# Kernel tuning notes

Hardware: AMD Instinct MI355X
Metric: run time of the kernel (lower is better)

Reference implementation:

```python
import jax, jax.numpy as jnp
import numpy as np

N, S, L, E, H = 8, 2, 512, 1024, 16
D = E // H  # head_dim = 64


def setup_inputs() -> dict:
    key = jax.random.key(0)
    ks = jax.random.split(key, 10)
    inp = {
        "values": jax.random.normal(ks[0], (N, S, L, E), dtype=jnp.float32),
        "keys": jax.random.normal(ks[1], (N, S, L, E), dtype=jnp.float32),
        "query": jax.random.normal(ks[2], (N, S, L, E), dtype=jnp.float32),
        "mask": jax.random.randint(ks[3], (N, S, L, 1), 0, 2, dtype=jnp.int32),
        # per-head projection weights, nn.Linear(D, D, bias=False): y = x @ W.T
        "Wv": jax.random.normal(ks[4], (D, D), dtype=jnp.float32) / np.sqrt(D),
        "Wk": jax.random.normal(ks[5], (D, D), dtype=jnp.float32) / np.sqrt(D),
        "Wq": jax.random.normal(ks[6], (D, D), dtype=jnp.float32) / np.sqrt(D),
        # output projection nn.Linear(E, E)
        "Wo": jax.random.normal(ks[7], (E, E), dtype=jnp.float32) / np.sqrt(E),
        "bo": jax.random.normal(ks[8], (E,), dtype=jnp.float32) * 0.01,
    }
    return inp


def reference(values, keys, query, mask, Wv, Wk, Wq, Wo, bo):
    n, s, l, e = query.shape
    h, d = H, D
    key_len = keys.shape[2]
    # split heads: (n, s, len, h, d)
    v = values.reshape(n, s, l, h, d) @ Wv.T
    k = keys.reshape(n, s, l, h, d) @ Wk.T
    q = query.reshape(n, s, l, h, d) @ Wq.T
    # energy: (n, s, h, q_len, k_len)
    energy = jnp.einsum('nsqhd,nskhd->nshqk', q, k)
    # mask[:, :, :, 0] masks QUERY positions (broadcast over heads and k)
    m = mask[:, :, :, 0]  # (n, s, l)
    energy = jnp.where(m[:, :, None, :, None] == 0, jnp.float32(-1e20), energy)
    # NOTE: softmax over the QUERY axis (dim=3), faithful to the original
    attn = jax.nn.softmax(energy / jnp.sqrt(jnp.float32(key_len)), axis=3)
    out = jnp.einsum('nshql,nslhd->nsqhd', attn, v)
    out = out.reshape(n, s, l, h * d)
    return out @ Wo.T + bo
```

## Files before the change

### kernel.cpp

```cpp
#include <hip/hip_runtime.h>
#include <math.h>

#define LL 512
#define EE 1024
#define HH 16
#define DD 64
#define NSX 16
#define NT (NSX*LL)
#define NSLE (NT*EE)
#define SCALE_Q 0.06375871f

typedef unsigned short u16;
typedef short bf16x8 __attribute__((ext_vector_type(8)));
typedef float f32x4 __attribute__((ext_vector_type(4)));

__device__ inline u16 f2bf(float f) {
  unsigned u = __float_as_uint(f);
  u += 0x7fff + ((u >> 16) & 1);
  return (u16)(u >> 16);
}

#define FEXP2(x) __builtin_amdgcn_exp2f(x)
#define MFMA32(a, b, c) __builtin_amdgcn_mfma_f32_16x16x32_bf16((a), (b), (c), 0, 0, 0)

__device__ inline void gload16(const void* g, void* l) {
  __builtin_amdgcn_global_load_lds(
      (const __attribute__((address_space(1))) unsigned int*)g,
      (__attribute__((address_space(3))) unsigned int*)l, 16, 0, 0);
}

__global__ void __launch_bounds__(256) convw_kernel(
    const float* __restrict__ Wv, const float* __restrict__ Wk,
    const float* __restrict__ Wq, const float* __restrict__ Wo,
    u16* __restrict__ Wvb, u16* __restrict__ Wkb,
    u16* __restrict__ Wqb, u16* __restrict__ Wob) {
  int i = blockIdx.x * 256 + threadIdx.x;
  const float* s; u16* d; int j;
  if (i < 262144) { s = Wo; d = Wob; j = i; }
  else {
    j = i - 262144;
    if (j < 1024)      { s = Wv; d = Wvb; }
    else if (j < 2048) { s = Wk; d = Wkb; j -= 1024; }
    else               { s = Wq; d = Wqb; j -= 2048; }
  }
  float4 f = ((const float4*)s)[j];
  ushort4 o; o.x = f2bf(f.x); o.y = f2bf(f.y); o.z = f2bf(f.z); o.w = f2bf(f.w);
  ((ushort4*)d)[j] = o;
}

__global__ void __launch_bounds__(256) proj_kernel(
    const float* __restrict__ vals, const float* __restrict__ keys,
    const float* __restrict__ qry,
    const u16* __restrict__ Wvb, const u16* __restrict__ Wkb,
    const u16* __restrict__ Wqb,
    u16* __restrict__ vpT, u16* __restrict__ kp, u16* __restrict__ qp) {
  const int b = blockIdx.x;
  const int tt0 = b & 7, hg = (b >> 3) & 3, ns = (b >> 5) & 15, mat = b >> 9;
  const int tid = threadIdx.x;
  const int wid = tid >> 6, lane = tid & 63, quad = lane >> 4, l16 = lane & 15;
  const int h = hg*4 + wid;
  const float* src = (mat == 0 ? vals : mat == 1 ? keys : qry);
  const u16*   W   = (mat == 0 ? Wvb  : mat == 1 ? Wkb  : Wqb);
  u16* dst = (mat == 1 ? kp : qp);
  const float sc = (mat == 2) ? SCALE_Q : 1.f;
  bf16x8 wf[4][2];
  #pragma unroll
  for (int nt = 0; nt < 4; ++nt) {
    wf[nt][0] = *(const bf16x8*)&W[(nt*16 + l16)*DD + quad*8];
    wf[nt][1] = *(const bf16x8*)&W[(nt*16 + l16)*DD + 32 + quad*8];
  }
  f32x4 z = {0.f, 0.f, 0.f, 0.f};
  const float* xr0 = src + (size_t)(ns*LL + tt0*16 + l16)*EE + h*DD;
  const float* xr1 = xr0 + (size_t)128*EE;
  float4 x0 = *(const float4*)&xr0[quad*8];
  float4 x1 = *(const float4*)&xr0[quad*8 + 4];
  float4 x2 = *(const float4*)&xr0[32 + quad*8];
  float4 x3 = *(const float4*)&xr0[32 + quad*8 + 4];
  float4 y0 = *(const float4*)&xr1[quad*8];
  float4 y1 = *(const float4*)&xr1[quad*8 + 4];
  float4 y2 = *(const float4*)&xr1[32 + quad*8];
  float4 y3 = *(const float4*)&xr1[32 + quad*8 + 4];
  #pragma unroll
  for (int j = 0; j < 4; ++j) {
    const int tt = tt0 + 8*j;
    const int t0 = ns*LL + tt*16;
    float4 n0, n1, n2, n3;
    if (j < 2) {
      const float* xrn = src + (size_t)(t0 + 256 + l16)*EE + h*DD;
      n0 = *(const float4*)&xrn[quad*8];
      n1 = *(const float4*)&xrn[quad*8 + 4];
      n2 = *(const float4*)&xrn[32 + quad*8];
      n3 = *(const float4*)&xrn[32 + quad*8 + 4];
    }
    bf16x8 af0, af1;
    af0[0] = (short)f2bf(x0.x); af0[1] = (short)f2bf(x0.y);
    af0[2] = (short)f2bf(x0.z); af0[3] = (short)f2bf(x0.w);
    af0[4] = (short)f2bf(x1.x); af0[5] = (short)f2bf(x1.y);
    af0[6] = (short)f2bf(x1.z); af0[7] = (short)f2bf(x1.w);
    af1[0] = (short)f2bf(x2.x); af1[1] = (short)f2bf(x2.y);
    af1[2] = (short)f2bf(x2.z); af1[3] = (short)f2bf(x2.w);
    af1[4] = (short)f2bf(x3.x); af1[5] = (short)f2bf(x3.y);
    af1[6] = (short)f2bf(x3.z); af1[7] = (short)f2bf(x3.w);
    if (mat == 0) {
      f32x4 acc[4];
      #pragma unroll
      for (int nt = 0; nt < 4; ++nt) {
        acc[nt] = MFMA32(af0, wf[nt][0], z);
        acc[nt] = MFMA32(af1, wf[nt][1], acc[nt]);
      }
      #pragma unroll
      for (int nt = 0; nt < 4; ++nt) {
        ushort4 o;
        o.x = f2bf(acc[nt][0]); o.y = f2bf(acc[nt][1]);
        o.z = f2bf(acc[nt][2]); o.w = f2bf(acc[nt][3]);
        size_t idx = ((size_t)((ns*HH + h)*DD + nt*16 + l16))*LL + tt*16 + quad*4;
        *(ushort4*)&vpT[idx] = o;
      }
    } else {
      f32x4 acc[4];
      #pragma unroll
      for (int nt = 0; nt < 4; ++nt) {
        acc[nt] = MFMA32(wf[nt][0], af0, z);
        acc[nt] = MFMA32(wf[nt][1], af1, acc[nt]);
      }
      #pragma unroll
      for (int nt = 0; nt < 4; ++nt) {
        ushort4 o;
        o.x = f2bf(acc[nt][0] * sc); o.y = f2bf(acc[nt][1] * sc);
        o.z = f2bf(acc[nt][2] * sc); o.w = f2bf(acc[nt][3] * sc);
        *(ushort4*)&dst[(size_t)(t0 + l16)*EE + h*DD + nt*16 + quad*4] = o;
      }
    }
    x0 = y0; x1 = y1; x2 = y2; x3 = y3;
    if (j < 2) { y0 = n0; y1 = n1; y2 = n2; y3 = n3; }
  }
}

__global__ void __launch_bounds__(1024, 4) attn_kernel(
    const u16* __restrict__ qp, const u16* __restrict__ kp,
    const u16* __restrict__ vpT, const int* __restrict__ mask,
    u16* __restrict__ oat) {
  const int b = blockIdx.x;
  const int h = b & 15, ns = b >> 4;
  const int tid = threadIdx.x;
  const int wid = tid >> 6, lane = tid & 63, quad = lane >> 4, l16 = lane & 15;
  __shared__ u16 Ks[LL][72];
  __shared__ u16 Vt[2][DD][72];
  __shared__ u16 pt[16][32][40];
  __shared__ float csum[LL];
  float* psum = (float*)pt;
  const size_t kgbase = ((size_t)(ns*LL))*EE + h*DD;
  for (int i = tid; i < 4096; i += 1024) {
    int row = i >> 3, seg = (i & 7) * 8;
    *(bf16x8*)&Ks[row][seg] = *(const bf16x8*)&kp[kgbase + (size_t)row*EE + seg];
  }
  const int q0 = wid*32;
  bf16x8 qf[2][2];
  float maf[2][4];
  #pragma unroll
  for (int qt = 0; qt < 2; ++qt) {
    const u16* qrow = qp + ((size_t)(ns*LL + q0 + qt*16 + l16))*EE + h*DD;
    qf[qt][0] = *(const bf16x8*)&qrow[quad*8];
    qf[qt][1] = *(const bf16x8*)&qrow[32 + quad*8];
    #pragma unroll
    for (int r = 0; r < 4; ++r)
      maf[qt][r] = mask[ns*LL + q0 + qt*16 + quad*4 + r] ? 1.f : 0.f;
  }
  f32x4 z = {0.f, 0.f, 0.f, 0.f};
  __syncthreads();
  for (int lt = 0; lt < 32; ++lt) {
    bf16x8 kf0 = *(const bf16x8*)&Ks[lt*16 + l16][quad*8];
    bf16x8 kf1 = *(const bf16x8*)&Ks[lt*16 + l16][32 + quad*8];
    float part = 0.f;
    #pragma unroll
    for (int qt = 0; qt < 2; ++qt) {
      __builtin_amdgcn_s_setprio(1);
      f32x4 e = MFMA32(qf[qt][0], kf0, z);
      e = MFMA32(qf[qt][1], kf1, e);
      __builtin_amdgcn_s_setprio(0);
      #pragma unroll
      for (int r = 0; r < 4; ++r)
        part += maf[qt][r] * FEXP2(e[r]);
    }
    part += __shfl_xor(part, 16);
    part += __shfl_xor(part, 32);
    if (quad == 0) psum[wid*512 + lt*16 + l16] = part;
  }
  __syncthreads();
  if (tid < LL) {
    float s = 0.f;
    #pragma unroll
    for (int w = 0; w < 16; ++w) s += psum[w*512 + tid];
    csum[tid] = (s > 0.f) ? 1.f/s : 0.f;
  }
  __syncthreads();
  f32x4 acc[4][2] = {{z,z},{z,z},{z,z},{z,z}};
  const size_t vgbase = ((size_t)((ns*HH + h)*DD))*LL;
  for (int lc = 0; lc < 8; ++lc) {
    if (tid < 512) {
      int row = tid >> 3, seg = (tid & 7) * 8;
      *(bf16x8*)&Vt[lc & 1][row][seg] =
          *(const bf16x8*)&vpT[vgbase + (size_t)row*LL + lc*64 + seg];
    }
    __syncthreads();
    #pragma unroll
    for (int lt2 = 0; lt2 < 4; ++lt2) {
      const int lrow = lc*64 + lt2*16 + l16;
      bf16x8 kf0 = *(const bf16x8*)&Ks[lrow][quad*8];
      bf16x8 kf1 = *(const bf16x8*)&Ks[lrow][32 + quad*8];
      const float csv = csum[lrow];
      #pragma unroll
      for (int qt = 0; qt < 2; ++qt) {
        __builtin_amdgcn_s_setprio(1);
        f32x4 e = MFMA32(qf[qt][0], kf0, z);
        e = MFMA32(qf[qt][1], kf1, e);
        __builtin_amdgcn_s_setprio(0);
        #pragma unroll
        for (int r = 0; r < 4; ++r)
          pt[wid][qt*16 + quad*4 + r][lt2 & 1 ? 16 + l16 : l16] =
              f2bf(maf[qt][r] * csv * FEXP2(e[r]));
        if (lt2 & 1) {
          bf16x8 pa = *(const bf16x8*)&pt[wid][qt*16 + l16][quad*8];
          __builtin_amdgcn_s_setprio(1);
          #pragma unroll
          for (int dt = 0; dt < 4; ++dt) {
            bf16x8 vb = *(const bf16x8*)&Vt[lc & 1][dt*16 + l16]
                                        [(lt2 >> 1)*32 + quad*8];
            acc[dt][qt] = MFMA32(pa, vb, acc[dt][qt]);
          }
          __builtin_amdgcn_s_setprio(0);
        }
      }
    }
  }
  #pragma unroll
  for (int qt = 0; qt < 2; ++qt)
    #pragma unroll
    for (int dt = 0; dt < 4; ++dt)
      #pragma unroll
      for (int r = 0; r < 4; ++r)
        oat[((size_t)(ns*LL + q0 + qt*16 + quad*4 + r))*EE + h*DD + dt*16 + l16] =
            f2bf(acc[dt][qt][r]);
}

__global__ void __launch_bounds__(256) out_gemm_kernel(
    const u16* __restrict__ A, const u16* __restrict__ Wob,
    const float* __restrict__ bo, float* __restrict__ Y) {
  __shared__ u16 As[128][64];
  __shared__ u16 Bs[128][64];
  const int b = blockIdx.x;
  const int nb = b & 7, mb = b >> 3;
  const int m0 = mb*128, n0 = nb*128;
  const int tid = threadIdx.x;
  const int wid = tid >> 6, lane = tid & 63, quad = lane >> 4, l16 = lane & 15;
  const int wm = (wid >> 1)*64, wn = (wid & 1)*64;
  const int r0 = tid >> 3, sseg = (tid & 7) * 8;
  u16* adst = &As[0][0] + tid*8;
  u16* bdst = &Bs[0][0] + tid*8;
  f32x4 z = {0.f, 0.f, 0.f, 0.f};
  f32x4 acc[4][4];
  #pragma unroll
  for (int i = 0; i < 4; ++i)
    #pragma unroll
    for (int j = 0; j < 4; ++j) acc[i][j] = z;
  for (int k0 = 0; k0 < EE; k0 += 64) {
    __syncthreads();
    #pragma unroll
    for (int it = 0; it < 4; ++it) {
      gload16(&A  [(size_t)(m0 + it*32 + r0)*EE + k0 + sseg], adst + it*2048);
      gload16(&Wob[(size_t)(n0 + it*32 + r0)*EE + k0 + sseg], bdst + it*2048);
    }
    __syncthreads();
    #pragma unroll
    for (int kk = 0; kk < 2; ++kk) {
      bf16x8 af[4], bfr[4];
      #pragma unroll
      for (int i = 0; i < 4; ++i)
        af[i] = *(const bf16x8*)&As[wm + i*16 + l16][kk*32 + quad*8];
      #pragma unroll
      for (int j = 0; j < 4; ++j)
        bfr[j] = *(const bf16x8*)&Bs[wn + j*16 + l16][kk*32 + quad*8];
      #pragma unroll
      for (int i = 0; i < 4; ++i)
        #pragma unroll
        for (int j = 0; j < 4; ++j)
          acc[i][j] = MFMA32(af[i], bfr[j], acc[i][j]);
    }
  }
  #pragma unroll
  for (int i = 0; i < 4; ++i)
    #pragma unroll
    for (int j = 0; j < 4; ++j) {
      int col = n0 + wn + j*16 + l16;
      float bias = bo[col];
      #pragma unroll
      for (int r = 0; r < 4; ++r)
        Y[(size_t)(m0 + wm + i*16 + quad*4 + r)*EE + col] = acc[i][j][r] + bias;
    }
}

extern "C" void kernel_launch(void* const* d_in, const int* in_sizes, int n_in,
                              void* d_out, int out_size, void* d_ws, size_t ws_size,
                              hipStream_t stream) {
  const float* values = (const float*)d_in[0];
  const float* keysp  = (const float*)d_in[1];
  const float* query  = (const float*)d_in[2];
  const int*   mask   = (const int*)d_in[3];
  const float* Wv = (const float*)d_in[4];
  const float* Wk = (const float*)d_in[5];
  const float* Wq = (const float*)d_in[6];
  const float* Wo = (const float*)d_in[7];
  const float* bo = (const float*)d_in[8];
  float* Y = (float*)d_out;

  u16* qp  = (u16*)d_ws;
  u16* kp  = qp + NSLE;
  u16* vpT = kp + NSLE;
  u16* oat = vpT + NSLE;
  u16* Wob = oat + NSLE;
  u16* Wvb = Wob + EE*EE;
  u16* Wkb = Wvb + DD*DD;
  u16* Wqb = Wkb + DD*DD;

  convw_kernel<<<1036, 256, 0, stream>>>(Wv, Wk, Wq, Wo, Wvb, Wkb, Wqb, Wob);
  proj_kernel<<<3*NSX*4*8, 256, 0, stream>>>(values, keysp, query,
                                             Wvb, Wkb, Wqb, vpT, kp, qp);
  attn_kernel<<<NSX*HH, 1024, 0, stream>>>(qp, kp, vpT, mask, oat);
  out_gemm_kernel<<<(NT/128)*(EE/128), 256, 0, stream>>>(oat, Wob, bo, Y);
}
```

Baseline: 232.8 us.

## Transpose score MFMA for vectorized P stores, drop setprio, shrink out-GEMM N tile

In the attention kernel, the second-pass score MFMA now has its operands swapped so each lane holds four consecutive key columns for one query row. This lets the probabilities be written to LDS as a single ushort4 and the column sums read as one float4, replacing scalar scattered stores. The s_setprio hints around the MFMAs are removed. The output GEMM tile shrinks from 128x128 to 128x64, doubling the block count (1024 blocks) to improve occupancy and CU coverage at the cost of more A-tile reloads.

```diff
diff --git a/kernel.cpp b/kernel.cpp
--- a/kernel.cpp
+++ b/kernel.cpp
@@ -157,6 +157,7 @@
   const int q0 = wid*32;
   bf16x8 qf[2][2];
   float maf[2][4];
+  float mqf[2];
   #pragma unroll
   for (int qt = 0; qt < 2; ++qt) {
     const u16* qrow = qp + ((size_t)(ns*LL + q0 + qt*16 + l16))*EE + h*DD;
@@ -165,6 +166,7 @@
     #pragma unroll
     for (int r = 0; r < 4; ++r)
       maf[qt][r] = mask[ns*LL + q0 + qt*16 + quad*4 + r] ? 1.f : 0.f;
+    mqf[qt] = mask[ns*LL + q0 + qt*16 + l16] ? 1.f : 0.f;
   }
   f32x4 z = {0.f, 0.f, 0.f, 0.f};
   __syncthreads();
@@ -174,10 +176,8 @@
     float part = 0.f;
     #pragma unroll
     for (int qt = 0; qt < 2; ++qt) {
-      __builtin_amdgcn_s_setprio(1);
       f32x4 e = MFMA32(qf[qt][0], kf0, z);
       e = MFMA32(qf[qt][1], kf1, e);
-      __builtin_amdgcn_s_setprio(0);
       #pragma unroll
       for (int r = 0; r < 4; ++r)
         part += maf[qt][r] * FEXP2(e[r]);
@@ -205,30 +205,29 @@
     __syncthreads();
     #pragma unroll
     for (int lt2 = 0; lt2 < 4; ++lt2) {
-      const int lrow = lc*64 + lt2*16 + l16;
-      bf16x8 kf0 = *(const bf16x8*)&Ks[lrow][quad*8];
-      bf16x8 kf1 = *(const bf16x8*)&Ks[lrow][32 + quad*8];
-      const float csv = csum[lrow];
+      const int lb = lc*64 + lt2*16;
+      bf16x8 kf0 = *(const bf16x8*)&Ks[lb + l16][quad*8];
+      bf16x8 kf1 = *(const bf16x8*)&Ks[lb + l16][32 + quad*8];
+      float4 cs4 = *(const float4*)&csum[lb + quad*4];
       #pragma unroll
       for (int qt = 0; qt < 2; ++qt) {
-        __builtin_amdgcn_s_setprio(1);
-        f32x4 e = MFMA32(qf[qt][0], kf0, z);
-        e = MFMA32(qf[qt][1], kf1, e);
-        __builtin_amdgcn_s_setprio(0);
-        #pragma unroll
-        for (int r = 0; r < 4; ++r)
-          pt[wid][qt*16 + quad*4 + r][lt2 & 1 ? 16 + l16 : l16] =
-              f2bf(maf[qt][r] * csv * FEXP2(e[r]));
+        f32x4 e = MFMA32(kf0, qf[qt][0], z);
+        e = MFMA32(kf1, qf[qt][1], e);
+        const float m = mqf[qt];
+        ushort4 o;
+        o.x = f2bf(m * cs4.x * FEXP2(e[0]));
+        o.y = f2bf(m * cs4.y * FEXP2(e[1]));
+        o.z = f2bf(m * cs4.z * FEXP2(e[2]));
+        o.w = f2bf(m * cs4.w * FEXP2(e[3]));
+        *(ushort4*)&pt[wid][qt*16 + l16][(lt2 & 1)*16 + quad*4] = o;
         if (lt2 & 1) {
           bf16x8 pa = *(const bf16x8*)&pt[wid][qt*16 + l16][quad*8];
-          __builtin_amdgcn_s_setprio(1);
           #pragma unroll
           for (int dt = 0; dt < 4; ++dt) {
             bf16x8 vb = *(const bf16x8*)&Vt[lc & 1][dt*16 + l16]
                                         [(lt2 >> 1)*32 + quad*8];
             acc[dt][qt] = MFMA32(pa, vb, acc[dt][qt]);
           }
-          __builtin_amdgcn_s_setprio(0);
         }
       }
     }
@@ -247,50 +246,51 @@
     const u16* __restrict__ A, const u16* __restrict__ Wob,
     const float* __restrict__ bo, float* __restrict__ Y) {
   __shared__ u16 As[128][64];
-  __shared__ u16 Bs[128][64];
+  __shared__ u16 Bs[64][64];
   const int b = blockIdx.x;
-  const int nb = b & 7, mb = b >> 3;
-  const int m0 = mb*128, n0 = nb*128;
+  const int nb = b & 15, mb = b >> 4;
+  const int m0 = mb*128, n0 = nb*64;
   const int tid = threadIdx.x;
   const int wid = tid >> 6, lane = tid & 63, quad = lane >> 4, l16 = lane & 15;
-  const int wm = (wid >> 1)*64, wn = (wid & 1)*64;
+  const int wm = (wid >> 1)*64, wn = (wid & 1)*32;
   const int r0 = tid >> 3, sseg = (tid & 7) * 8;
   u16* adst = &As[0][0] + tid*8;
   u16* bdst = &Bs[0][0] + tid*8;
   f32x4 z = {0.f, 0.f, 0.f, 0.f};
-  f32x4 acc[4][4];
+  f32x4 acc[4][2];
   #pragma unroll
   for (int i = 0; i < 4; ++i)
     #pragma unroll
-    for (int j = 0; j < 4; ++j) acc[i][j] = z;
+    for (int j = 0; j < 2; ++j) acc[i][j] = z;
   for (int k0 = 0; k0 < EE; k0 += 64) {
     __syncthreads();
     #pragma unroll
-    for (int it = 0; it < 4; ++it) {
-      gload16(&A  [(size_t)(m0 + it*32 + r0)*EE + k0 + sseg], adst + it*2048);
+    for (int it = 0; it < 4; ++it)
+      gload16(&A[(size_t)(m0 + it*32 + r0)*EE + k0 + sseg], adst + it*2048);
+    #pragma unroll
+    for (int it = 0; it < 2; ++it)
       gload16(&Wob[(size_t)(n0 + it*32 + r0)*EE + k0 + sseg], bdst + it*2048);
-    }
     __syncthreads();
     #pragma unroll
     for (int kk = 0; kk < 2; ++kk) {
-      bf16x8 af[4], bfr[4];
+      bf16x8 af[4], bfr[2];
       #pragma unroll
       for (int i = 0; i < 4; ++i)
         af[i] = *(const bf16x8*)&As[wm + i*16 + l16][kk*32 + quad*8];
       #pragma unroll
-      for (int j = 0; j < 4; ++j)
+      for (int j = 0; j < 2; ++j)
         bfr[j] = *(const bf16x8*)&Bs[wn + j*16 + l16][kk*32 + quad*8];
       #pragma unroll
       for (int i = 0; i < 4; ++i)
         #pragma unroll
-        for (int j = 0; j < 4; ++j)
+        for (int j = 0; j < 2; ++j)
           acc[i][j] = MFMA32(af[i], bfr[j], acc[i][j]);
     }
   }
   #pragma unroll
   for (int i = 0; i < 4; ++i)
     #pragma unroll
-    for (int j = 0; j < 4; ++j) {
+    for (int j = 0; j < 2; ++j) {
       int col = n0 + wn + j*16 + l16;
       float bias = bo[col];
       #pragma unroll
@@ -326,5 +326,5 @@
   proj_kernel<<<3*NSX*4*8, 256, 0, stream>>>(values, keysp, query,
                                              Wvb, Wkb, Wqb, vpT, kp, qp);
   attn_kernel<<<NSX*HH, 1024, 0, stream>>>(qp, kp, vpT, mask, oat);
-  out_gemm_kernel<<<(NT/128)*(EE/128), 256, 0, stream>>>(oat, Wob, bo, Y);
-}
+  out_gemm_kernel<<<(NT/128)*(EE/64), 256, 0, stream>>>(oat, Wob, bo, Y);
+}
```

Measured after the change: 230.7 us. No clear change (-0.9%).
